# Kernel optimization log

Hardware: AMD Instinct MI355X
Metric: run time of the kernel (lower is better)

The kernel has to match this reference:

```python
import jax, jax.numpy as jnp
import numpy as np

UNITS, ORDER, THETA, DT = 512, 256, 784.0, 1.0


def _lmu_AB(order, theta, dt):
    # Continuous-time Legendre delay system (Voelker & Eliasmith 2018)
    Q = np.arange(order, dtype=np.float64)
    R = (2.0 * Q + 1.0)[:, None] / theta
    i, j = np.meshgrid(Q, Q, indexing='ij')
    A = np.where(i < j, -1.0, (-1.0) ** (i - j + 1)) * R
    B = ((-1.0) ** Q)[:, None] * R
    # ZOH discretization: Ad = expm(A*dt); Bd = A^{-1}(Ad - I)B
    Ad = np.asarray(jax.scipy.linalg.expm(jnp.asarray(A * dt, dtype=jnp.float64)))
    Bd = np.linalg.solve(A, (Ad - np.eye(order)) @ B)
    # cell stores AT = (Ad - I)^T so that m <- m + m@AT + u@BT
    return (Ad - np.eye(order)).T.astype(np.float32), Bd.T.astype(np.float32)


def setup_inputs() -> dict:
    key = jax.random.key(0)
    ks = jax.random.split(key, 6)
    D = 1
    x = jax.random.normal(ks[0], (64, 1024, D), dtype=jnp.float32)
    # lecun_uniform: U(-sqrt(3/fan_in), sqrt(3/fan_in))
    ie = jax.random.uniform(ks[1], (D, 1), minval=-np.sqrt(3.0 / D), maxval=np.sqrt(3.0 / D), dtype=jnp.float32)
    he = jax.random.uniform(ks[2], (UNITS, 1), minval=-np.sqrt(3.0 / UNITS), maxval=np.sqrt(3.0 / UNITS), dtype=jnp.float32)
    me = jnp.zeros((ORDER, 1), dtype=jnp.float32)  # Constant(0) initializer
    # glorot_normal: std = sqrt(2/(fan_in+fan_out))
    ik = jax.random.normal(ks[3], (D, UNITS), dtype=jnp.float32) * np.sqrt(2.0 / (D + UNITS))
    hk = jax.random.normal(ks[4], (UNITS, UNITS), dtype=jnp.float32) * np.sqrt(2.0 / (2 * UNITS))
    mk = jax.random.normal(ks[5], (ORDER, UNITS), dtype=jnp.float32) * np.sqrt(2.0 / (ORDER + UNITS))
    AT, BT = _lmu_AB(ORDER, THETA / DT, DT)
    return {"x": x, "input_encoders": ie, "hidden_encoders": he, "memory_encoders": me,
            "input_kernel": ik, "hidden_kernel": hk, "memory_kernel": mk,
            "AT": jnp.asarray(AT), "BT": jnp.asarray(BT)}


def reference(x, input_encoders, hidden_encoders, memory_encoders,
              input_kernel, hidden_kernel, memory_kernel, AT, BT):
    B = x.shape[0]
    h0 = jnp.zeros((B, UNITS), dtype=x.dtype)
    m0 = jnp.zeros((B, ORDER), dtype=x.dtype)

    def step(carry, xt):  # xt: [B, D]
        h, m = carry
        u = xt @ input_encoders + h @ hidden_encoders + m @ memory_encoders  # [B,1]
        m = m + m @ AT + u @ BT                                             # [B,order]
        h = jnp.tanh(xt @ input_kernel + h @ hidden_kernel + m @ memory_kernel)
        return (h, m), h

    xs = jnp.transpose(x, (1, 0, 2))  # [T,B,D]
    _, hs = jax.lax.scan(step, (h0, m0), xs)
    return jnp.transpose(hs, (1, 0, 2))  # [B,T,units]
```

## Files before the change

kernel.cpp:

```cpp
#include <hip/hip_runtime.h>
#include <hip/hip_fp16.h>

typedef unsigned int u32;
typedef unsigned short u16;
typedef _Float16 half2v __attribute__((ext_vector_type(2)));

#define N_UNITS 512
#define N_ORDER 256
#define N_T     1024
#define N_B     64
#define KWG     4
#define PKT_STRIDE 288

__device__ inline float dot2f(u32 a, u32 b, float acc) {
    return __builtin_amdgcn_fdot2(__builtin_bit_cast(half2v, a),
                                  __builtin_bit_cast(half2v, b), acc, false);
}
__device__ inline u16 f2h_bits(float v) {
    _Float16 f = (_Float16)v;
    return __builtin_bit_cast(u16, f);
}
__device__ inline float hbits2f(u32 dw) {
    u16 s = (u16)(dw & 0xFFFFu);
    _Float16 f = __builtin_bit_cast(_Float16, s);
    return (float)f;
}
__device__ inline u32 pack_h2(float a, float b) {
    return (u32)f2h_bits(a) | ((u32)f2h_bits(b) << 16);
}
__device__ inline u32 aload(const u32* p) {
    return __hip_atomic_load(p, __ATOMIC_RELAXED, __HIP_MEMORY_SCOPE_AGENT);
}
__device__ inline void astore(u32* p, u32 v) {
    __hip_atomic_store(p, v, __ATOMIC_RELAXED, __HIP_MEMORY_SCOPE_AGENT);
}

__global__ __launch_bounds__(256)
void prep_hk(const float* __restrict__ hk, u32* __restrict__ hk2) {
    int tid = blockIdx.x * 256 + threadIdx.x;
    int kk = tid >> 9, c = tid & 511;
    hk2[tid] = pack_h2(hk[(2 * kk) * 512 + c], hk[(2 * kk + 1) * 512 + c]);
}

__global__ __launch_bounds__(512)
void prep_amk(const float* __restrict__ mk, const float* __restrict__ at,
              const float* __restrict__ bt,
              u32* __restrict__ amk2, float* __restrict__ bmk) {
    int bj = blockIdx.x, c = threadIdx.x;
    if (bj < 128) {
        int j0 = 2 * bj, j1 = j0 + 1;
        float a0 = mk[j0 * 512 + c];
        float a1 = mk[j1 * 512 + c];
        #pragma unroll 8
        for (int k = 0; k < 256; ++k) {
            float w = mk[k * 512 + c];
            a0 = fmaf(at[j0 * 256 + k], w, a0);
            a1 = fmaf(at[j1 * 256 + k], w, a1);
        }
        amk2[bj * 512 + c] = pack_h2(a0, a1);
    } else {
        float s = 0.f;
        #pragma unroll 8
        for (int k = 0; k < 256; ++k) s = fmaf(bt[k], mk[k * 512 + c], s);
        bmk[c] = s;
    }
}

__global__ __launch_bounds__(512, 2)
void lmu_main(const float* __restrict__ x, const float* __restrict__ ie,
              const float* __restrict__ he, const float* __restrict__ me,
              const float* __restrict__ ik, const float* __restrict__ bt,
              const float* __restrict__ at,
              const u32* __restrict__ hk2, const u32* __restrict__ amk2,
              const float* __restrict__ bmk,
              u32* __restrict__ pkt, float* __restrict__ out) {
    __shared__ float xs[N_T];
    __shared__ float he_sl[128], ik_sl[128], bmk_sl[128];
    __shared__ float me_sl[64], bt_sl[64];
    __shared__ __align__(8) u16 h_h16[N_UNITS];
    __shared__ __align__(8) u16 m_hi16[N_ORDER], m_lo16[N_ORDER];
    __shared__ __align__(8) float mf[N_ORDER];
    __shared__ float zbuf[512], ampart[512];
    __shared__ float upart[4];
    __shared__ float upw[2];

    const int tid = threadIdx.x;
    const int g   = blockIdx.x;
    const int b   = g & 63;
    const int q   = g >> 6;
    const int kg  = tid >> 7;
    const int cl  = tid & 127;
    const int kg8 = tid >> 6;
    const int jl  = tid & 63;
    const int J   = 64 * q + jl;
    const int lane = tid & 63;

    for (int i = tid; i < N_T; i += 512) xs[i] = x[b * N_T + i];
    if (tid < 128) {
        he_sl[tid]  = he[128 * q + tid];
        ik_sl[tid]  = ik[128 * q + tid];
        bmk_sl[tid] = bmk[128 * q + tid];
    }
    if (tid < 64) { me_sl[tid] = me[J]; bt_sl[tid] = bt[J]; }
    h_h16[tid] = 0;
    if (tid < 256) { m_hi16[tid] = 0; m_lo16[tid] = 0; mf[tid] = 0.f; }
    if (tid < 4) upart[tid] = 0.f;
    const float ie0 = ie[0];

    u32 hk_w[64];
    #pragma unroll
    for (int i = 0; i < 64; ++i)
        hk_w[i] = hk2[(size_t)(64 * kg + i) * 512 + 128 * q + cl];
    u32 amk_w[32];
    #pragma unroll
    for (int i = 0; i < 32; ++i)
        amk_w[i] = amk2[(size_t)(32 * kg + i) * 512 + 128 * q + cl];
    float at_w[32];
    #pragma unroll
    for (int i = 0; i < 32; ++i)
        at_w[i] = at[(size_t)(32 * kg8 + i) * 256 + J];

    __syncthreads();

    const u32* h2u   = reinterpret_cast<const u32*>(h_h16);
    const u32* m_hi2 = reinterpret_cast<const u32*>(m_hi16);
    const u32* m_lo2 = reinterpret_cast<const u32*>(m_lo16);
    float* outb = out + (size_t)b * N_T * N_UNITS;

    for (int t = 0; t < N_T; ++t) {
        if (t > 0) {
            const u32 ep  = (u32)t;
            const int par = (t - 1) & 1;
            if (tid < 195) {
                int pi = (tid < 192) ? (tid >> 6) : (tid - 192);
                int q2 = pi + (pi >= q ? 1 : 0);
                const u32* base = pkt + (size_t)(par * 256 + b * 4 + q2) * PKT_STRIDE;
                if (tid < 192) {
                    int i = tid & 63;
                    u32 d0, d1, d2, d3;
                    for (;;) {
                        d0 = aload(base + 4 * i + 0);
                        d1 = aload(base + 4 * i + 1);
                        d2 = aload(base + 4 * i + 2);
                        d3 = aload(base + 4 * i + 3);
                        if (((((d0 >> 16) ^ ep) | ((d1 >> 16) ^ ep)) |
                             (((d2 >> 16) ^ ep) | ((d3 >> 16) ^ ep))) == 0) break;
                    }
                    if (i < 32) {
                        int idx = 64 * q2 + 2 * i;
                        mf[idx]         = hbits2f(d0) + hbits2f(d1);
                        m_hi16[idx]     = (u16)d0;  m_lo16[idx]     = (u16)d1;
                        mf[idx + 1]     = hbits2f(d2) + hbits2f(d3);
                        m_hi16[idx + 1] = (u16)d2;  m_lo16[idx + 1] = (u16)d3;
                    } else {
                        int idx = 128 * q2 + (4 * i - 128);
                        h_h16[idx]     = (u16)d0;
                        h_h16[idx + 1] = (u16)d1;
                        h_h16[idx + 2] = (u16)d2;
                        h_h16[idx + 3] = (u16)d3;
                    }
                } else {
                    u32 d0, d1;
                    for (;;) {
                        d0 = aload(base + 256);
                        d1 = aload(base + 257);
                        if ((((d0 >> 16) ^ ep) | ((d1 >> 16) ^ ep)) == 0) break;
                    }
                    upart[q2] = hbits2f(d0) + hbits2f(d1);
                }
            }
        }
        __syncthreads();

        {
            float z = 0.f;
            #pragma unroll
            for (int i = 0; i < 64; ++i)
                z = dot2f(h2u[64 * kg + i], hk_w[i], z);
            #pragma unroll
            for (int i = 0; i < 32; ++i) {
                u32 w = amk_w[i];
                z = dot2f(m_hi2[32 * kg + i], w, z);
                z = dot2f(m_lo2[32 * kg + i], w, z);
            }
            zbuf[tid] = z;
            float am = 0.f;
            #pragma unroll
            for (int i = 0; i < 32; ++i)
                am = fmaf(mf[32 * kg8 + i], at_w[i], am);
            ampart[tid] = am;
        }
        __syncthreads();

        float u = 0.f, mnew = 0.f, hnew = 0.f;
        u16 mhi_b = 0, mlo_b = 0;
        if (tid < 128)
            u = upart[0] + upart[1] + upart[2] + upart[3] + xs[t] * ie0;
        if (tid < 64) {
            mnew = mf[J] + u * bt_sl[tid];
            #pragma unroll
            for (int gi = 0; gi < 8; ++gi) mnew += ampart[tid + 64 * gi];
            _Float16 hi = (_Float16)mnew;
            float lo = mnew - (float)hi;
            mhi_b = __builtin_bit_cast(u16, hi);
            mlo_b = f2h_bits(lo);
            mf[J] = mnew;
            m_hi16[J] = mhi_b;
            m_lo16[J] = mlo_b;
        }
        if (tid < 128) {
            float zf = zbuf[tid] + zbuf[tid + 128] + zbuf[tid + 256] + zbuf[tid + 384]
                     + xs[t] * ik_sl[tid] + u * bmk_sl[tid];
            hnew = tanhf(zf);
            outb[(size_t)t * N_UNITS + 128 * q + tid] = hnew;
            h_h16[128 * q + tid] = f2h_bits(hnew);
        }

        if (t < N_T - 1) {
            const u32 eph = (u32)(t + 1) << 16;
            u32* myb = pkt + (size_t)((t & 1) * 256 + b * 4 + q) * PKT_STRIDE;
            if (tid < 64) {
                astore(myb + 2 * tid,     (u32)mhi_b | eph);
                astore(myb + 2 * tid + 1, (u32)mlo_b | eph);
            }
            if (tid < 128)
                astore(myb + 128 + tid, (u32)f2h_bits(hnew) | eph);

            float up = 0.f;
            if (tid < 128) {
                up = hnew * he_sl[tid];
                if (tid < 64) up = fmaf(mnew, me_sl[tid], up);
            }
            #pragma unroll
            for (int off = 32; off > 0; off >>= 1) up += __shfl_down(up, off);
            if (lane == 0 && tid < 128) upw[tid >> 6] = up;
            __syncthreads();
            if (tid == 0) {
                float myu = upw[0] + upw[1];
                upart[q] = myu;
                _Float16 hi = (_Float16)myu;
                float lo = myu - (float)hi;
                astore(myb + 256, (u32)__builtin_bit_cast(u16, hi) | eph);
                astore(myb + 257, (u32)f2h_bits(lo) | eph);
            }
        }
    }
}

extern "C" void kernel_launch(void* const* d_in, const int* in_sizes, int n_in,
                              void* d_out, int out_size, void* d_ws, size_t ws_size,
                              hipStream_t stream) {
    const float* x  = (const float*)d_in[0];
    const float* ie = (const float*)d_in[1];
    const float* he = (const float*)d_in[2];
    const float* me = (const float*)d_in[3];
    const float* ik = (const float*)d_in[4];
    const float* hk = (const float*)d_in[5];
    const float* mk = (const float*)d_in[6];
    const float* at = (const float*)d_in[7];
    const float* bt = (const float*)d_in[8];

    u32*   hk2  = (u32*)d_ws;
    u32*   amk2 = hk2 + 256 * 512;
    float* bmk  = (float*)(amk2 + 128 * 512);
    u32*   pkt  = (u32*)(bmk + 512);

    prep_hk<<<512, 256, 0, stream>>>(hk, hk2);
    prep_amk<<<129, 512, 0, stream>>>(mk, at, bt, amk2, bmk);
    lmu_main<<<N_B * KWG, 512, 0, stream>>>(x, ie, he, me, ik, bt, at,
                                            hk2, amk2, bmk, pkt, (float*)d_out);
}
```

Measured before the change: 2.903 ms.

## Remove per-step barrier by splitting u partials across waves, vectorize LDS reads

The u reduction is now split into three per-wave partial fragments (two h waves, one m wave), each published directly by its wave, which removes the extra __syncthreads and single-thread combine per timestep. The m update moves to a separate wave (tid 128..191) and keeps its state in a register. LDS reads in the dot products switch to uint4/float4 with multiple accumulators, and tanhf is replaced by an exp-based fast tanh. Accuracy of tanh and the changed summation order may slightly alter results, and more packet words must be polled per peer.

```diff
diff --git a/kernel.cpp b/kernel.cpp
--- a/kernel.cpp
+++ b/kernel.cpp
@@ -33,6 +33,15 @@
 }
 __device__ inline void astore(u32* p, u32 v) {
     __hip_atomic_store(p, v, __ATOMIC_RELAXED, __HIP_MEMORY_SCOPE_AGENT);
+}
+__device__ inline float tanh_fast(float x) {
+    float xa = fminf(fmaxf(x, -12.f), 12.f);
+    float e  = __expf(2.f * xa);
+#if __has_builtin(__builtin_amdgcn_rcpf)
+    return (e - 1.f) * __builtin_amdgcn_rcpf(e + 1.f);
+#else
+    return (e - 1.f) / (e + 1.f);
+#endif
 }
 
 __global__ __launch_bounds__(256)
@@ -77,12 +86,11 @@
     __shared__ float xs[N_T];
     __shared__ float he_sl[128], ik_sl[128], bmk_sl[128];
     __shared__ float me_sl[64], bt_sl[64];
-    __shared__ __align__(8) u16 h_h16[N_UNITS];
-    __shared__ __align__(8) u16 m_hi16[N_ORDER], m_lo16[N_ORDER];
-    __shared__ __align__(8) float mf[N_ORDER];
+    __shared__ __align__(16) u16 h_h16[N_UNITS];
+    __shared__ __align__(16) u16 m_hi16[N_ORDER], m_lo16[N_ORDER];
+    __shared__ __align__(16) float mf[N_ORDER];
+    __shared__ __align__(16) float ufrag[12];
     __shared__ float zbuf[512], ampart[512];
-    __shared__ float upart[4];
-    __shared__ float upw[2];
 
     const int tid = threadIdx.x;
     const int g   = blockIdx.x;
@@ -104,7 +112,7 @@
     if (tid < 64) { me_sl[tid] = me[J]; bt_sl[tid] = bt[J]; }
     h_h16[tid] = 0;
     if (tid < 256) { m_hi16[tid] = 0; m_lo16[tid] = 0; mf[tid] = 0.f; }
-    if (tid < 4) upart[tid] = 0.f;
+    if (tid < 12) ufrag[tid] = 0.f;
     const float ie0 = ie[0];
 
     u32 hk_w[64];
@@ -119,129 +127,184 @@
     #pragma unroll
     for (int i = 0; i < 32; ++i)
         at_w[i] = at[(size_t)(32 * kg8 + i) * 256 + J];
+    #pragma unroll
+    for (int i = 0; i < 64; ++i) asm volatile("" : "+v"(hk_w[i]));
+    #pragma unroll
+    for (int i = 0; i < 32; ++i) asm volatile("" : "+v"(amk_w[i]));
+    #pragma unroll
+    for (int i = 0; i < 32; ++i) asm volatile("" : "+v"(at_w[i]));
 
     __syncthreads();
 
-    const u32* h2u   = reinterpret_cast<const u32*>(h_h16);
-    const u32* m_hi2 = reinterpret_cast<const u32*>(m_hi16);
-    const u32* m_lo2 = reinterpret_cast<const u32*>(m_lo16);
+    const uint4*  h4   = reinterpret_cast<const uint4*>(h_h16);
+    const uint4*  mh4  = reinterpret_cast<const uint4*>(m_hi16);
+    const uint4*  ml4  = reinterpret_cast<const uint4*>(m_lo16);
+    const float4* mfv4 = reinterpret_cast<const float4*>(mf);
+    const float4* ufv4 = reinterpret_cast<const float4*>(ufrag);
     float* outb = out + (size_t)b * N_T * N_UNITS;
 
+    float mreg = 0.f;
+
     for (int t = 0; t < N_T; ++t) {
-        if (t > 0) {
+        if (t > 0 && tid < 198) {
             const u32 ep  = (u32)t;
             const int par = (t - 1) & 1;
-            if (tid < 195) {
-                int pi = (tid < 192) ? (tid >> 6) : (tid - 192);
+            if (tid < 192) {
+                int pi = tid >> 6, i = tid & 63;
                 int q2 = pi + (pi >= q ? 1 : 0);
                 const u32* base = pkt + (size_t)(par * 256 + b * 4 + q2) * PKT_STRIDE;
-                if (tid < 192) {
-                    int i = tid & 63;
-                    u32 d0, d1, d2, d3;
+                u32 d0, d1, d2, d3;
+                if (i < 32) {
+                    const u32* p4 = base + 4 * i;
                     for (;;) {
-                        d0 = aload(base + 4 * i + 0);
-                        d1 = aload(base + 4 * i + 1);
-                        d2 = aload(base + 4 * i + 2);
-                        d3 = aload(base + 4 * i + 3);
+                        d0 = aload(p4 + 0); d1 = aload(p4 + 1);
+                        d2 = aload(p4 + 2); d3 = aload(p4 + 3);
                         if (((((d0 >> 16) ^ ep) | ((d1 >> 16) ^ ep)) |
                              (((d2 >> 16) ^ ep) | ((d3 >> 16) ^ ep))) == 0) break;
                     }
-                    if (i < 32) {
-                        int idx = 64 * q2 + 2 * i;
-                        mf[idx]         = hbits2f(d0) + hbits2f(d1);
-                        m_hi16[idx]     = (u16)d0;  m_lo16[idx]     = (u16)d1;
-                        mf[idx + 1]     = hbits2f(d2) + hbits2f(d3);
-                        m_hi16[idx + 1] = (u16)d2;  m_lo16[idx + 1] = (u16)d3;
-                    } else {
-                        int idx = 128 * q2 + (4 * i - 128);
-                        h_h16[idx]     = (u16)d0;
-                        h_h16[idx + 1] = (u16)d1;
-                        h_h16[idx + 2] = (u16)d2;
-                        h_h16[idx + 3] = (u16)d3;
+                    int w = 32 * q2 + i;
+                    *reinterpret_cast<float2*>(&mf[2 * w]) =
+                        make_float2(hbits2f(d0) + hbits2f(d1),
+                                    hbits2f(d2) + hbits2f(d3));
+                    reinterpret_cast<u32*>(m_hi16)[w] = (d0 & 0xFFFFu) | (d2 << 16);
+                    reinterpret_cast<u32*>(m_lo16)[w] = (d1 & 0xFFFFu) | (d3 << 16);
+                } else {
+                    const u32* p4 = base + 128 + 4 * (i - 32);
+                    for (;;) {
+                        d0 = aload(p4 + 0); d1 = aload(p4 + 1);
+                        d2 = aload(p4 + 2); d3 = aload(p4 + 3);
+                        if (((((d0 >> 16) ^ ep) | ((d1 >> 16) ^ ep)) |
+                             (((d2 >> 16) ^ ep) | ((d3 >> 16) ^ ep))) == 0) break;
                     }
+                    int w = 64 * q2 + 2 * (i - 32);
+                    uint2 hv;
+                    hv.x = (d0 & 0xFFFFu) | (d1 << 16);
+                    hv.y = (d2 & 0xFFFFu) | (d3 << 16);
+                    *reinterpret_cast<uint2*>(&reinterpret_cast<u32*>(h_h16)[w]) = hv;
+                }
+            } else {
+                int r = tid - 192;
+                int pi = r >> 1, sub = r & 1;
+                int q2 = pi + (pi >= q ? 1 : 0);
+                const u32* base =
+                    pkt + (size_t)(par * 256 + b * 4 + q2) * PKT_STRIDE + 256;
+                if (sub == 0) {
+                    u32 d0, d1, d2, d3;
+                    for (;;) {
+                        d0 = aload(base + 0); d1 = aload(base + 1);
+                        d2 = aload(base + 2); d3 = aload(base + 3);
+                        if (((((d0 >> 16) ^ ep) | ((d1 >> 16) ^ ep)) |
+                             (((d2 >> 16) ^ ep) | ((d3 >> 16) ^ ep))) == 0) break;
+                    }
+                    ufrag[3 * q2 + 0] = hbits2f(d0) + hbits2f(d1);
+                    ufrag[3 * q2 + 1] = hbits2f(d2) + hbits2f(d3);
                 } else {
                     u32 d0, d1;
                     for (;;) {
-                        d0 = aload(base + 256);
-                        d1 = aload(base + 257);
+                        d0 = aload(base + 4); d1 = aload(base + 5);
                         if ((((d0 >> 16) ^ ep) | ((d1 >> 16) ^ ep)) == 0) break;
                     }
-                    upart[q2] = hbits2f(d0) + hbits2f(d1);
+                    ufrag[3 * q2 + 2] = hbits2f(d0) + hbits2f(d1);
                 }
             }
         }
         __syncthreads();
 
+        float u;
         {
-            float z = 0.f;
-            #pragma unroll
-            for (int i = 0; i < 64; ++i)
-                z = dot2f(h2u[64 * kg + i], hk_w[i], z);
-            #pragma unroll
-            for (int i = 0; i < 32; ++i) {
-                u32 w = amk_w[i];
-                z = dot2f(m_hi2[32 * kg + i], w, z);
-                z = dot2f(m_lo2[32 * kg + i], w, z);
-            }
-            zbuf[tid] = z;
-            float am = 0.f;
-            #pragma unroll
-            for (int i = 0; i < 32; ++i)
-                am = fmaf(mf[32 * kg8 + i], at_w[i], am);
-            ampart[tid] = am;
+            float4 fa = ufv4[0], fb = ufv4[1], fc = ufv4[2];
+            u = ((fa.x + fa.y) + (fa.z + fa.w)) + ((fb.x + fb.y) + (fb.z + fb.w))
+              + ((fc.x + fc.y) + (fc.z + fc.w)) + xs[t] * ie0;
+        }
+
+        {
+            float z0 = 0.f, z1 = 0.f, z2 = 0.f, z3 = 0.f;
+            #pragma unroll
+            for (int j = 0; j < 16; ++j) {
+                uint4 hv = h4[16 * kg + j];
+                z0 = dot2f(hv.x, hk_w[4 * j + 0], z0);
+                z1 = dot2f(hv.y, hk_w[4 * j + 1], z1);
+                z2 = dot2f(hv.z, hk_w[4 * j + 2], z2);
+                z3 = dot2f(hv.w, hk_w[4 * j + 3], z3);
+            }
+            #pragma unroll
+            for (int j = 0; j < 8; ++j) {
+                uint4 mh = mh4[8 * kg + j];
+                uint4 ml = ml4[8 * kg + j];
+                z0 = dot2f(mh.x, amk_w[4 * j + 0], z0);
+                z1 = dot2f(mh.y, amk_w[4 * j + 1], z1);
+                z2 = dot2f(mh.z, amk_w[4 * j + 2], z2);
+                z3 = dot2f(mh.w, amk_w[4 * j + 3], z3);
+                z0 = dot2f(ml.x, amk_w[4 * j + 0], z0);
+                z1 = dot2f(ml.y, amk_w[4 * j + 1], z1);
+                z2 = dot2f(ml.z, amk_w[4 * j + 2], z2);
+                z3 = dot2f(ml.w, amk_w[4 * j + 3], z3);
+            }
+            zbuf[tid] = (z0 + z1) + (z2 + z3);
+            float a0 = 0.f, a1 = 0.f;
+            #pragma unroll
+            for (int j = 0; j < 8; ++j) {
+                float4 mv = mfv4[8 * kg8 + j];
+                a0 = fmaf(mv.x, at_w[4 * j + 0], a0);
+                a1 = fmaf(mv.y, at_w[4 * j + 1], a1);
+                a0 = fmaf(mv.z, at_w[4 * j + 2], a0);
+                a1 = fmaf(mv.w, at_w[4 * j + 3], a1);
+            }
+            ampart[tid] = a0 + a1;
         }
         __syncthreads();
 
-        float u = 0.f, mnew = 0.f, hnew = 0.f;
-        u16 mhi_b = 0, mlo_b = 0;
-        if (tid < 128)
-            u = upart[0] + upart[1] + upart[2] + upart[3] + xs[t] * ie0;
-        if (tid < 64) {
-            mnew = mf[J] + u * bt_sl[tid];
-            #pragma unroll
-            for (int gi = 0; gi < 8; ++gi) mnew += ampart[tid + 64 * gi];
-            _Float16 hi = (_Float16)mnew;
-            float lo = mnew - (float)hi;
-            mhi_b = __builtin_bit_cast(u16, hi);
-            mlo_b = f2h_bits(lo);
-            mf[J] = mnew;
-            m_hi16[J] = mhi_b;
-            m_lo16[J] = mlo_b;
-        }
+        const bool pub = (t < N_T - 1);
+        const u32 eph = (u32)(t + 1) << 16;
+        u32* myb = pkt + (size_t)((t & 1) * 256 + b * 4 + q) * PKT_STRIDE;
+
         if (tid < 128) {
             float zf = zbuf[tid] + zbuf[tid + 128] + zbuf[tid + 256] + zbuf[tid + 384]
                      + xs[t] * ik_sl[tid] + u * bmk_sl[tid];
-            hnew = tanhf(zf);
+            float hnew = tanh_fast(zf);
+            u16 hb = f2h_bits(hnew);
+            if (pub) astore(myb + 128 + tid, (u32)hb | eph);
+            h_h16[128 * q + tid] = hb;
             outb[(size_t)t * N_UNITS + 128 * q + tid] = hnew;
-            h_h16[128 * q + tid] = f2h_bits(hnew);
-        }
-
-        if (t < N_T - 1) {
-            const u32 eph = (u32)(t + 1) << 16;
-            u32* myb = pkt + (size_t)((t & 1) * 256 + b * 4 + q) * PKT_STRIDE;
-            if (tid < 64) {
-                astore(myb + 2 * tid,     (u32)mhi_b | eph);
-                astore(myb + 2 * tid + 1, (u32)mlo_b | eph);
-            }
-            if (tid < 128)
-                astore(myb + 128 + tid, (u32)f2h_bits(hnew) | eph);
-
-            float up = 0.f;
-            if (tid < 128) {
-                up = hnew * he_sl[tid];
-                if (tid < 64) up = fmaf(mnew, me_sl[tid], up);
-            }
+            float up = hnew * he_sl[tid];
             #pragma unroll
             for (int off = 32; off > 0; off >>= 1) up += __shfl_down(up, off);
-            if (lane == 0 && tid < 128) upw[tid >> 6] = up;
-            __syncthreads();
-            if (tid == 0) {
-                float myu = upw[0] + upw[1];
-                upart[q] = myu;
-                _Float16 hi = (_Float16)myu;
-                float lo = myu - (float)hi;
-                astore(myb + 256, (u32)__builtin_bit_cast(u16, hi) | eph);
-                astore(myb + 257, (u32)f2h_bits(lo) | eph);
+            if (lane == 0) {
+                int w = tid >> 6;
+                ufrag[3 * q + w] = up;
+                if (pub) {
+                    _Float16 hi = (_Float16)up;
+                    float lo = up - (float)hi;
+                    astore(myb + 256 + 2 * w,     (u32)__builtin_bit_cast(u16, hi) | eph);
+                    astore(myb + 256 + 2 * w + 1, (u32)f2h_bits(lo) | eph);
+                }
+            }
+        } else if (tid < 192) {
+            float mnew = mreg + u * bt_sl[jl];
+            #pragma unroll
+            for (int gi = 0; gi < 8; ++gi) mnew += ampart[jl + 64 * gi];
+            mreg = mnew;
+            _Float16 hi = (_Float16)mnew;
+            float lo = mnew - (float)hi;
+            u16 hib = __builtin_bit_cast(u16, hi), lob = f2h_bits(lo);
+            mf[J] = mnew;
+            m_hi16[J] = hib;
+            m_lo16[J] = lob;
+            if (pub) {
+                astore(myb + 2 * jl,     (u32)hib | eph);
+                astore(myb + 2 * jl + 1, (u32)lob | eph);
+            }
+            float up = mnew * me_sl[jl];
+            #pragma unroll
+            for (int off = 32; off > 0; off >>= 1) up += __shfl_down(up, off);
+            if (lane == 0) {
+                ufrag[3 * q + 2] = up;
+                if (pub) {
+                    _Float16 uhi = (_Float16)up;
+                    float ulo = up - (float)uhi;
+                    astore(myb + 260, (u32)__builtin_bit_cast(u16, uhi) | eph);
+                    astore(myb + 261, (u32)f2h_bits(ulo) | eph);
+                }
             }
         }
     }
```

Result: no change. 2.959 ms (+1.9%).
